# Performance work log

Hardware: AMD Instinct MI355X
Metric: run time of the kernel (lower is better)

Reference implementation:

```python
import jax, jax.numpy as jnp
import numpy as np

B, C, H, W = 16, 256, 56, 56
G, K, R = 16, 3, 2
CR = C // R          # reduced channels = 128
KKG = K * K * G      # span output channels = 144
EPS = 1e-5


def setup_inputs() -> dict:
    key = jax.random.key(0)
    ks = jax.random.split(key, 5)
    return {
        "x": jax.random.normal(ks[0], (B, C, H, W), jnp.float32),
        "w_reduce": jax.random.normal(ks[1], (CR, C), jnp.float32) * 0.05,
        "b_reduce": jax.random.normal(ks[2], (CR,), jnp.float32) * 0.05,
        "gamma": jnp.ones((CR,), jnp.float32),
        "beta": jnp.zeros((CR,), jnp.float32),
        "w_span": jax.random.normal(ks[3], (KKG, CR), jnp.float32) * 0.05,
        "b_span": jax.random.normal(ks[4], (KKG,), jnp.float32) * 0.05,
    }


def _conv1x1(x, w, bias):
    # 1x1 conv == channel contraction
    return jnp.einsum('bchw,oc->bohw', x, w) + bias[None, :, None, None]


def _involution(x, w_reduce, b_reduce, gamma, beta, w_span, b_span):
    b, c, h, w = x.shape
    # kernel-generation branch: reduce -> BN (batch stats) -> ReLU -> span
    t = _conv1x1(x, w_reduce, b_reduce)
    mu = t.mean(axis=(0, 2, 3), keepdims=True)
    var = t.var(axis=(0, 2, 3), keepdims=True)  # biased, as torch BN training
    t = (t - mu) * jax.lax.rsqrt(var + EPS)
    t = t * gamma[None, :, None, None] + beta[None, :, None, None]
    t = jax.nn.relu(t)
    kern = _conv1x1(t, w_span, b_span)  # [b, k*k*g, h, w]
    # 'b (k j g) h w -> b g (k j) h w'
    kern = kern.reshape(b, K, K, G, h, w).transpose(0, 3, 1, 2, 4, 5)
    kern = kern.reshape(b, G, K * K, h, w)
    # unfold x into [b, g, d, k*k, h, w] via shifted padded slices (no dense im2col buffer write pattern beyond necessity)
    p = K // 2
    xp = jnp.pad(x, ((0, 0), (0, 0), (p, p), (p, p)))
    patches = jnp.stack(
        [xp[:, :, i:i + h, j:j + w] for i in range(K) for j in range(K)],
        axis=2)  # [b, c, k*k, h, w]
    patches = patches.reshape(b, G, c // G, K * K, h, w)
    out = jnp.einsum('bgdxhw,bgxhw->bgdhw', patches, kern)  # weighted window sum
    return out.reshape(b, c, h, w)


def reference(x, w_reduce, b_reduce, gamma, beta, w_span, b_span):
    return _involution(x, w_reduce, b_reduce, gamma, beta, w_span, b_span)
```

## Files before the change

### kernel.cpp

```cpp
#include <hip/hip_runtime.h>

#define B_   16
#define C_   256
#define HW_  3136
#define W_   56
#define CR_  128
#define KKG_ 144
#define G_   16
#define NPOS (B_*HW_)
#define EPS_ 1e-5f
#define NBLK 784

typedef float f32x4 __attribute__((ext_vector_type(4)));
typedef short s16x8 __attribute__((ext_vector_type(8)));

#define T2_OFF_B    0
#define KERN_OFF_B  12845056
#define GACC_OFF_B  27295744
#define WBFR_OFF_B  27296768
#define WBFS_OFF_B  27362304

__device__ inline unsigned short f2bf(float f) {
    unsigned u = __float_as_uint(f);
    u += 0x7fff + ((u >> 16) & 1);
    return (unsigned short)(u >> 16);
}
__device__ inline float bf2f(unsigned short h) {
    return __uint_as_float(((unsigned)h) << 16);
}
__device__ inline unsigned pk2(float a, float b) {
    return (unsigned)f2bf(a) | ((unsigned)f2bf(b) << 16);
}

__global__ __launch_bounds__(256) void prep_cast(
    const float* __restrict__ w_reduce, const float* __restrict__ w_span,
    unsigned short* __restrict__ wbfr, unsigned short* __restrict__ wbfs,
    float* __restrict__ gacc)
{
    int idx = blockIdx.x * 256 + threadIdx.x;
    if (idx < 256) gacc[idx] = 0.0f;
    if (idx < 32768) {
        wbfr[idx] = f2bf(w_reduce[idx]);
    } else {
        int k = idx - 32768;
        if (k < 18432) wbfs[k] = f2bf(w_span[k]);
    }
}

__global__ __launch_bounds__(256) void reduce_mfma(
    const float* __restrict__ x, const unsigned short* __restrict__ wbfr,
    unsigned short* __restrict__ t2, float* __restrict__ gacc)
{
    __shared__ float redp[128][2], redq[128][2];

    const int tid = threadIdx.x;
    const int lane = tid & 63, wv = tid >> 6;
    const int q = lane >> 4, i = lane & 15;
    const int mrow = (wv >> 1) * 64, nrow = (wv & 1) * 32;
    const int blk = blockIdx.x;
    const int b = blk / 49;
    const int p0 = (blk % 49) * 64;

    const float* xpl = x + (size_t)b * C_ * HW_ + p0 + nrow + i;
    const unsigned short* wb = wbfr + (size_t)(mrow + i) * C_ + q * 8;

    f32x4 acc[4][2] = {};

    #pragma unroll
    for (int c0 = 0; c0 < C_; c0 += 32) {
        s16x8 af[4];
        #pragma unroll
        for (int mt = 0; mt < 4; mt++)
            af[mt] = *(const s16x8*)(wb + (size_t)mt * 16 * C_ + c0);

        s16x8 bfr[2];
        #pragma unroll
        for (int nt = 0; nt < 2; nt++) {
            const float* xc = xpl + nt * 16;
            union { s16x8 v; unsigned u[4]; } Bv;
            #pragma unroll
            for (int k2 = 0; k2 < 4; k2++) {
                float fa = xc[(size_t)(c0 + q * 8 + 2 * k2) * HW_];
                float fb = xc[(size_t)(c0 + q * 8 + 2 * k2 + 1) * HW_];
                Bv.u[k2] = pk2(fa, fb);
            }
            bfr[nt] = Bv.v;
        }

        #pragma unroll
        for (int mt = 0; mt < 4; mt++)
            #pragma unroll
            for (int nt = 0; nt < 2; nt++)
                acc[mt][nt] = __builtin_amdgcn_mfma_f32_16x16x32_bf16(
                    af[mt], bfr[nt], acc[mt][nt], 0, 0, 0);
    }

    #pragma unroll
    for (int mt = 0; mt < 4; mt++) {
        #pragma unroll
        for (int nt = 0; nt < 2; nt++) {
            int p = p0 + nrow + nt * 16 + i;
            uint2 pr;
            pr.x = pk2(acc[mt][nt][0], acc[mt][nt][1]);
            pr.y = pk2(acc[mt][nt][2], acc[mt][nt][3]);
            *(uint2*)(t2 + ((size_t)b * HW_ + p) * CR_ + mrow + mt * 16 + q * 4) = pr;
        }
        #pragma unroll
        for (int reg = 0; reg < 4; reg++) {
            float v0 = acc[mt][0][reg], v1 = acc[mt][1][reg];
            float s = v0 + v1;
            float ss = v0 * v0 + v1 * v1;
            #pragma unroll
            for (int m = 1; m < 16; m <<= 1) {
                s  += __shfl_xor(s, m);
                ss += __shfl_xor(ss, m);
            }
            if (i == 0) {
                int o = mrow + mt * 16 + q * 4 + reg;
                redp[o][wv & 1] = s;
                redq[o][wv & 1] = ss;
            }
        }
    }
    __syncthreads();
    if (tid < 128) atomicAdd(&gacc[tid], redp[tid][0] + redp[tid][1]);
    else           atomicAdd(&gacc[tid], redq[tid - 128][0] + redq[tid - 128][1]);
}

__global__ __launch_bounds__(256) void span_mfma(
    const unsigned short* __restrict__ t2, const unsigned short* __restrict__ wbfs,
    const float* __restrict__ b_span, const float* __restrict__ gacc,
    const float* __restrict__ gamma, const float* __restrict__ beta,
    unsigned short* __restrict__ kern)
{
    __shared__ __align__(16) float scs[128], shs[128];
    __shared__ float bsp[144];

    const int tid = threadIdx.x;
    const int lane = tid & 63, wv = tid >> 6;
    const int q = lane >> 4, i = lane & 15;
    const int blk = blockIdx.x;
    const int b = blk / 49;
    const int p0 = (blk % 49) * 64;

    if (tid < 128) {
        float s = gacc[tid], ss = gacc[128 + tid];
        const float inv_n = 1.0f / (float)NPOS;
        float mu = s * inv_n;
        float var = ss * inv_n - mu * mu;
        float sc = gamma[tid] * rsqrtf(var + EPS_);
        scs[tid] = sc;
        shs[tid] = beta[tid] - mu * sc;
    }
    if (tid < 144) bsp[tid] = b_span[tid];
    __syncthreads();

    const int p = p0 + wv * 16 + i;
    const unsigned short* tb = t2 + ((size_t)b * HW_ + p) * CR_ + q * 8;
    const unsigned short* wb = wbfs + (size_t)i * CR_ + q * 8;

    f32x4 acc[9] = {};

    #pragma unroll
    for (int c0 = 0; c0 < CR_; c0 += 32) {
        const int cb = c0 + q * 8;
        s16x8 traw = *(const s16x8*)(tb + c0);
        float4 s0 = *(const float4*)&scs[cb];
        float4 s1 = *(const float4*)&scs[cb + 4];
        float4 h0 = *(const float4*)&shs[cb];
        float4 h1 = *(const float4*)&shs[cb + 4];
        float f0 = fmaxf(fmaf(bf2f((unsigned short)traw[0]), s0.x, h0.x), 0.f);
        float f1 = fmaxf(fmaf(bf2f((unsigned short)traw[1]), s0.y, h0.y), 0.f);
        float f2 = fmaxf(fmaf(bf2f((unsigned short)traw[2]), s0.z, h0.z), 0.f);
        float f3 = fmaxf(fmaf(bf2f((unsigned short)traw[3]), s0.w, h0.w), 0.f);
        float f4 = fmaxf(fmaf(bf2f((unsigned short)traw[4]), s1.x, h1.x), 0.f);
        float f5 = fmaxf(fmaf(bf2f((unsigned short)traw[5]), s1.y, h1.y), 0.f);
        float f6 = fmaxf(fmaf(bf2f((unsigned short)traw[6]), s1.z, h1.z), 0.f);
        float f7 = fmaxf(fmaf(bf2f((unsigned short)traw[7]), s1.w, h1.w), 0.f);
        union { s16x8 v; unsigned u[4]; } Bv;
        Bv.u[0] = pk2(f0, f1);
        Bv.u[1] = pk2(f2, f3);
        Bv.u[2] = pk2(f4, f5);
        Bv.u[3] = pk2(f6, f7);

        #pragma unroll
        for (int mt = 0; mt < 9; mt++) {
            s16x8 af = *(const s16x8*)(wb + (size_t)mt * 16 * CR_ + c0);
            acc[mt] = __builtin_amdgcn_mfma_f32_16x16x32_bf16(af, Bv.v, acc[mt], 0, 0, 0);
        }
    }

    #pragma unroll
    for (int mt = 0; mt < 9; mt++) {
        #pragma unroll
        for (int reg = 0; reg < 4; reg++) {
            int o2 = mt * 16 + q * 4 + reg;
            kern[((size_t)b * KKG_ + o2) * HW_ + p] = f2bf(acc[mt][reg] + bsp[o2]);
        }
    }
}

__global__ __launch_bounds__(256) void involution_apply(
    const float* __restrict__ x, const unsigned short* __restrict__ kern,
    float* __restrict__ out)
{
    int gtid = blockIdx.x * 256 + threadIdx.x;
    int pix = gtid % HW_;
    int bg  = gtid / HW_;
    int g = bg & 15;
    int b = bg >> 4;
    int h = pix / W_;
    int w = pix % W_;

    const unsigned short* kb = kern + (size_t)b * KKG_ * HW_ + pix;
    float kv[9];
    #pragma unroll
    for (int kk = 0; kk < 9; kk++)
        kv[kk] = bf2f(kb[(size_t)(kk * G_ + g) * HW_]);

    float acc[16];
    #pragma unroll
    for (int d = 0; d < 16; d++) acc[d] = 0.0f;

    const float* xb = x + (size_t)(b * C_ + g * 16) * HW_;
    #pragma unroll
    for (int di = 0; di < 3; di++) {
        int hh = h + di - 1;
        if (hh < 0 || hh >= W_) continue;
        #pragma unroll
        for (int dj = 0; dj < 3; dj++) {
            int ww = w + dj - 1;
            if (ww < 0 || ww >= W_) continue;
            float kval = kv[di * 3 + dj];
            int off = hh * W_ + ww;
            #pragma unroll
            for (int d = 0; d < 16; d++)
                acc[d] = fmaf(xb[(size_t)d * HW_ + off], kval, acc[d]);
        }
    }
    float* ob = out + (size_t)(b * C_ + g * 16) * HW_ + pix;
    #pragma unroll
    for (int d = 0; d < 16; d++) ob[(size_t)d * HW_] = acc[d];
}

extern "C" void kernel_launch(void* const* d_in, const int* in_sizes, int n_in,
                              void* d_out, int out_size, void* d_ws, size_t ws_size,
                              hipStream_t stream) {
    const float* x        = (const float*)d_in[0];
    const float* w_reduce = (const float*)d_in[1];
    const float* gamma    = (const float*)d_in[3];
    const float* beta     = (const float*)d_in[4];
    const float* w_span   = (const float*)d_in[5];
    const float* b_span   = (const float*)d_in[6];
    float* out = (float*)d_out;

    char* wsb = (char*)d_ws;
    unsigned short* t2   = (unsigned short*)(wsb + T2_OFF_B);
    unsigned short* kern = (unsigned short*)(wsb + KERN_OFF_B);
    float*          gacc = (float*)(wsb + GACC_OFF_B);
    unsigned short* wbfr = (unsigned short*)(wsb + WBFR_OFF_B);
    unsigned short* wbfs = (unsigned short*)(wsb + WBFS_OFF_B);

    prep_cast<<<200, 256, 0, stream>>>(w_reduce, w_span, wbfr, wbfs, gacc);
    reduce_mfma<<<NBLK, 256, 0, stream>>>(x, wbfr, t2, gacc);
    span_mfma<<<NBLK, 256, 0, stream>>>(t2, wbfs, b_span, gacc, gamma, beta, kern);
    involution_apply<<<(B_ * G_ * HW_) / 256, 256, 0, stream>>>(x, kern, out);
}
```

Baseline: 191.2 us.

## Stage reduce and span GEMM inputs through LDS with async double-buffered loads

The reduce and span GEMM kernels now load their activation tiles into shared memory with global_load_lds and double-buffer across channel chunks. The reduce tile uses an XOR swizzle. This replaces strided per-lane global reads of x and t2 with coalesced 16-byte loads that overlap with the MFMA work. The change also switches to the packed hardware bf16 conversion, adds a minimum of 3 blocks per CU to the launch bounds, and reorders the generated kernel rows to [b,g,kk] so the apply kernel reads contiguous planes. The cost is extra barriers per chunk and more shared memory per block, which may limit occupancy.

```diff
diff --git a/kernel.cpp b/kernel.cpp
--- a/kernel.cpp
+++ b/kernel.cpp
@@ -1,4 +1,5 @@
 #include <hip/hip_runtime.h>
+#include <hip/hip_bf16.h>
 
 #define B_   16
 #define C_   256
@@ -28,8 +29,17 @@
 __device__ inline float bf2f(unsigned short h) {
     return __uint_as_float(((unsigned)h) << 16);
 }
-__device__ inline unsigned pk2(float a, float b) {
-    return (unsigned)f2bf(a) | ((unsigned)f2bf(b) << 16);
+__device__ inline unsigned pkcvt(float a, float b) {
+    float2 f2; f2.x = a; f2.y = b;
+    __hip_bfloat162 h = __float22bfloat162_rn(f2);
+    union { __hip_bfloat162 h2; unsigned u; } cv; cv.h2 = h;
+    return cv.u;
+}
+
+typedef const __attribute__((address_space(1))) unsigned int* gas_t;
+typedef __attribute__((address_space(3))) unsigned int* las_t;
+__device__ inline void gload_lds16(const void* g, void* l) {
+    __builtin_amdgcn_global_load_lds((gas_t)g, (las_t)l, 16, 0, 0);
 }
 
 __global__ __launch_bounds__(256) void prep_cast(
@@ -47,10 +57,11 @@
     }
 }
 
-__global__ __launch_bounds__(256) void reduce_mfma(
+__global__ __launch_bounds__(256, 3) void reduce_mfma(
     const float* __restrict__ x, const unsigned short* __restrict__ wbfr,
     unsigned short* __restrict__ t2, float* __restrict__ gacc)
 {
+    __shared__ __align__(16) float xbuf[2][2048];
     __shared__ float redp[128][2], redq[128][2];
 
     const int tid = threadIdx.x;
@@ -61,38 +72,67 @@
     const int b = blk / 49;
     const int p0 = (blk % 49) * 64;
 
-    const float* xpl = x + (size_t)b * C_ * HW_ + p0 + nrow + i;
+    const float* xb = x + (size_t)b * C_ * HW_ + p0;
     const unsigned short* wb = wbfr + (size_t)(mrow + i) * C_ + q * 8;
 
+    int c_s[2], pq_s[2];
+    #pragma unroll
+    for (int e = 0; e < 2; e++) {
+        int U = e * 256 + tid;
+        int c = U >> 4;
+        c_s[e] = c;
+        pq_s[e] = (U & 15) ^ ((c >> 1) & 7);
+    }
+    const int ldsb = (tid & ~63) * 4;
+
     f32x4 acc[4][2] = {};
 
     #pragma unroll
-    for (int c0 = 0; c0 < C_; c0 += 32) {
+    for (int e = 0; e < 2; e++)
+        gload_lds16(xb + (size_t)c_s[e] * HW_ + pq_s[e] * 4,
+                    &xbuf[0][e * 1024 + ldsb]);
+    __syncthreads();
+
+    #pragma unroll
+    for (int ch = 0; ch < 8; ch++) {
+        const int cur = ch & 1;
+        if (ch < 7) {
+            const float* xc = xb + (size_t)(ch + 1) * 32 * HW_;
+            #pragma unroll
+            for (int e = 0; e < 2; e++)
+                gload_lds16(xc + (size_t)c_s[e] * HW_ + pq_s[e] * 4,
+                            &xbuf[cur ^ 1][e * 1024 + ldsb]);
+        }
+        const int c0 = ch * 32;
         s16x8 af[4];
         #pragma unroll
         for (int mt = 0; mt < 4; mt++)
             af[mt] = *(const s16x8*)(wb + (size_t)mt * 16 * C_ + c0);
 
+        const float* bufc = xbuf[cur];
         s16x8 bfr[2];
         #pragma unroll
         for (int nt = 0; nt < 2; nt++) {
-            const float* xc = xpl + nt * 16;
+            const int p = nrow + nt * 16 + i;
+            const int pq = p >> 2, pm = p & 3;
             union { s16x8 v; unsigned u[4]; } Bv;
             #pragma unroll
             for (int k2 = 0; k2 < 4; k2++) {
-                float fa = xc[(size_t)(c0 + q * 8 + 2 * k2) * HW_];
-                float fb = xc[(size_t)(c0 + q * 8 + 2 * k2 + 1) * HW_];
-                Bv.u[k2] = pk2(fa, fb);
+                int cc = q * 8 + 2 * k2;
+                int u0 = cc * 16 + (pq ^ ((cc >> 1) & 7));
+                float fa = bufc[u0 * 4 + pm];
+                float fb = bufc[u0 * 4 + 64 + pm];
+                Bv.u[k2] = pkcvt(fa, fb);
             }
             bfr[nt] = Bv.v;
         }
-
         #pragma unroll
         for (int mt = 0; mt < 4; mt++)
             #pragma unroll
             for (int nt = 0; nt < 2; nt++)
                 acc[mt][nt] = __builtin_amdgcn_mfma_f32_16x16x32_bf16(
                     af[mt], bfr[nt], acc[mt][nt], 0, 0, 0);
+        __syncthreads();
     }
 
     #pragma unroll
@@ -101,8 +141,8 @@
         for (int nt = 0; nt < 2; nt++) {
             int p = p0 + nrow + nt * 16 + i;
             uint2 pr;
-            pr.x = pk2(acc[mt][nt][0], acc[mt][nt][1]);
-            pr.y = pk2(acc[mt][nt][2], acc[mt][nt][3]);
+            pr.x = pkcvt(acc[mt][nt][0], acc[mt][nt][1]);
+            pr.y = pkcvt(acc[mt][nt][2], acc[mt][nt][3]);
             *(uint2*)(t2 + ((size_t)b * HW_ + p) * CR_ + mrow + mt * 16 + q * 4) = pr;
         }
         #pragma unroll
@@ -127,14 +167,14 @@
     else           atomicAdd(&gacc[tid], redq[tid - 128][0] + redq[tid - 128][1]);
 }
 
-__global__ __launch_bounds__(256) void span_mfma(
+__global__ __launch_bounds__(256, 3) void span_mfma(
     const unsigned short* __restrict__ t2, const unsigned short* __restrict__ wbfs,
     const float* __restrict__ b_span, const float* __restrict__ gacc,
     const float* __restrict__ gamma, const float* __restrict__ beta,
     unsigned short* __restrict__ kern)
 {
-    __shared__ __align__(16) float scs[128], shs[128];
-    __shared__ float bsp[144];
+    __shared__ __align__(16) unsigned short tbuf[2][2048];
+    __shared__ float scs[128], shs[128], bsp[144];
 
     const int tid = threadIdx.x;
     const int lane = tid & 63, wv = tid >> 6;
@@ -153,49 +193,53 @@
         shs[tid] = beta[tid] - mu * sc;
     }
     if (tid < 144) bsp[tid] = b_span[tid];
+
+    const unsigned short* trow =
+        t2 + ((size_t)b * HW_ + p0 + (tid >> 2)) * CR_ + (tid & 3) * 8;
+    const int ldsb = (tid & ~63) * 8;
+    const int ufr = ((wv * 16 + i) * 4 + q) * 8;
+    const unsigned short* wb = wbfs + (size_t)i * CR_ + q * 8;
+
+    f32x4 acc[9] = {};
+
     __syncthreads();
-
-    const int p = p0 + wv * 16 + i;
-    const unsigned short* tb = t2 + ((size_t)b * HW_ + p) * CR_ + q * 8;
-    const unsigned short* wb = wbfs + (size_t)i * CR_ + q * 8;
-
-    f32x4 acc[9] = {};
-
-    #pragma unroll
-    for (int c0 = 0; c0 < CR_; c0 += 32) {
+    gload_lds16(trow, &tbuf[0][ldsb]);
+    __syncthreads();
+
+    #pragma unroll
+    for (int ch = 0; ch < 4; ch++) {
+        const int cur = ch & 1;
+        if (ch < 3)
+            gload_lds16(trow + (ch + 1) * 32, &tbuf[cur ^ 1][ldsb]);
+
+        const int c0 = ch * 32;
         const int cb = c0 + q * 8;
-        s16x8 traw = *(const s16x8*)(tb + c0);
-        float4 s0 = *(const float4*)&scs[cb];
-        float4 s1 = *(const float4*)&scs[cb + 4];
-        float4 h0 = *(const float4*)&shs[cb];
-        float4 h1 = *(const float4*)&shs[cb + 4];
-        float f0 = fmaxf(fmaf(bf2f((unsigned short)traw[0]), s0.x, h0.x), 0.f);
-        float f1 = fmaxf(fmaf(bf2f((unsigned short)traw[1]), s0.y, h0.y), 0.f);
-        float f2 = fmaxf(fmaf(bf2f((unsigned short)traw[2]), s0.z, h0.z), 0.f);
-        float f3 = fmaxf(fmaf(bf2f((unsigned short)traw[3]), s0.w, h0.w), 0.f);
-        float f4 = fmaxf(fmaf(bf2f((unsigned short)traw[4]), s1.x, h1.x), 0.f);
-        float f5 = fmaxf(fmaf(bf2f((unsigned short)traw[5]), s1.y, h1.y), 0.f);
-        float f6 = fmaxf(fmaf(bf2f((unsigned short)traw[6]), s1.z, h1.z), 0.f);
-        float f7 = fmaxf(fmaf(bf2f((unsigned short)traw[7]), s1.w, h1.w), 0.f);
+        s16x8 raw = *(const s16x8*)&tbuf[cur][ufr];
+        float f[8];
+        #pragma unroll
+        for (int k = 0; k < 8; k++)
+            f[k] = fmaxf(fmaf(bf2f((unsigned short)raw[k]),
+                              scs[cb + k], shs[cb + k]), 0.0f);
         union { s16x8 v; unsigned u[4]; } Bv;
-        Bv.u[0] = pk2(f0, f1);
-        Bv.u[1] = pk2(f2, f3);
-        Bv.u[2] = pk2(f4, f5);
-        Bv.u[3] = pk2(f6, f7);
+        #pragma unroll
+        for (int k2 = 0; k2 < 4; k2++) Bv.u[k2] = pkcvt(f[2*k2], f[2*k2+1]);
 
         #pragma unroll
         for (int mt = 0; mt < 9; mt++) {
             s16x8 af = *(const s16x8*)(wb + (size_t)mt * 16 * CR_ + c0);
             acc[mt] = __builtin_amdgcn_mfma_f32_16x16x32_bf16(af, Bv.v, acc[mt], 0, 0, 0);
         }
-    }
-
+        __syncthreads();
+    }
+
+    const int p = p0 + wv * 16 + i;
     #pragma unroll
     for (int mt = 0; mt < 9; mt++) {
         #pragma unroll
         for (int reg = 0; reg < 4; reg++) {
             int o2 = mt * 16 + q * 4 + reg;
-            kern[((size_t)b * KKG_ + o2) * HW_ + p] = f2bf(acc[mt][reg] + bsp[o2]);
+            int row = (o2 & 15) * 9 + (o2 >> 4);
+            kern[((size_t)b * KKG_ + row) * HW_ + p] = f2bf(acc[mt][reg] + bsp[o2]);
         }
     }
 }
@@ -212,11 +256,11 @@
     int h = pix / W_;
     int w = pix % W_;
 
-    const unsigned short* kb = kern + (size_t)b * KKG_ * HW_ + pix;
+    const unsigned short* kb = kern + ((size_t)(b * G_ + g) * 9) * HW_ + pix;
     float kv[9];
     #pragma unroll
     for (int kk = 0; kk < 9; kk++)
-        kv[kk] = bf2f(kb[(size_t)(kk * G_ + g) * HW_]);
+        kv[kk] = bf2f(kb[(size_t)kk * HW_]);
 
     float acc[16];
     #pragma unroll
```

Result: faster. 185.3 us (-3.1%).
